# Performance work log

Measured on AMD Instinct MI355X. Metric: run time of the kernel, lower is better.

The kernel has to match this reference:

```python
import jax, jax.numpy as jnp
import numpy as np

EPS = 1e-5

def ln(x, g, b):
    m = x.mean(-1, keepdims=True)
    v = x.var(-1, keepdims=True)
    return (x - m) / jnp.sqrt(v + EPS) * g + b

def setup_inputs() -> dict:
    key = jax.random.key(0)
    ks = jax.random.split(key, 16)
    def p(k, shape, fan):
        return jax.random.normal(k, shape, jnp.float32) * (1.0 / np.sqrt(fan))
    B, N, M = 4, 256, 256
    C = 256
    inp = {}
    inp["tracks"] = jax.random.normal(ks[0], (B, 1028, N), jnp.float32)
    inp["detections"] = jax.random.normal(ks[1], (B, 1028, M), jnp.float32)
    # app encoder: Linear(1024,256) -> LN -> ReLU -> Linear(256,256)
    inp["wa1"] = p(ks[2], (1024, C), 1024); inp["ba1"] = jnp.zeros((C,), jnp.float32)
    inp["gla"] = jnp.ones((C,), jnp.float32); inp["bla"] = jnp.zeros((C,), jnp.float32)
    inp["wa2"] = p(ks[3], (C, C), C); inp["ba2"] = jnp.zeros((C,), jnp.float32)
    # geo encoder: Linear(4,128) -> LN -> ReLU -> Linear(128,256)
    inp["wg1"] = p(ks[4], (4, C // 2), 4); inp["bg1"] = jnp.zeros((C // 2,), jnp.float32)
    inp["glg"] = jnp.ones((C // 2,), jnp.float32); inp["blg"] = jnp.zeros((C // 2,), jnp.float32)
    inp["wg2"] = p(ks[5], (C // 2, C), C // 2); inp["bg2"] = jnp.zeros((C,), jnp.float32)
    # fusion LayerNorm
    inp["gf"] = jnp.ones((C,), jnp.float32); inp["bf"] = jnp.zeros((C,), jnp.float32)
    # cross-attention (4 heads, head_dim 64)
    inp["wq"] = p(ks[6], (C, C), C); inp["bq"] = jnp.zeros((C,), jnp.float32)
    inp["wk"] = p(ks[7], (C, C), C); inp["bk"] = jnp.zeros((C,), jnp.float32)
    inp["wv"] = p(ks[8], (C, C), C); inp["bv"] = jnp.zeros((C,), jnp.float32)
    inp["wo"] = p(ks[9], (C, C), C); inp["bo"] = jnp.zeros((C,), jnp.float32)
    # classifier: Linear(512,128) -> ReLU -> Linear(128,1)
    inp["wc1"] = p(ks[10], (2 * C, 128), 2 * C); inp["bc1"] = jnp.zeros((128,), jnp.float32)
    inp["wc2"] = p(ks[11], (128, 1), 128); inp["bc2"] = jnp.zeros((1,), jnp.float32)
    return inp

def reference(tracks, detections, wa1, ba1, gla, bla, wa2, ba2,
              wg1, bg1, glg, blg, wg2, bg2, gf, bf,
              wq, bq, wk, bk, wv, bv, wo, bo,
              wc1, bc1, wc2, bc2):
    tr = tracks.transpose(0, 2, 1)       # (B, N, 1028)
    de = detections.transpose(0, 2, 1)   # (B, M, 1028)

    def encode(x):
        app, geo = x[..., :1024], x[..., 1024:]
        h = jax.nn.relu(ln(app @ wa1 + ba1, gla, bla)) @ wa2 + ba2
        g = jax.nn.relu(ln(geo @ wg1 + bg1, glg, blg)) @ wg2 + bg2
        return ln(h + g, gf, bf)

    t_emb = encode(tr)   # (B, N, C)
    d_emb = encode(de)   # (B, M, C)

    B, N, C = t_emb.shape
    M = d_emb.shape[1]
    H, dh = 4, C // 4

    # Cross-attention (computed in the original forward but its output is never used)
    q = (t_emb @ wq + bq).reshape(B, N, H, dh)
    k = (d_emb @ wk + bk).reshape(B, M, H, dh)
    v = (d_emb @ wv + bv).reshape(B, M, H, dh)
    att = jax.nn.softmax(jnp.einsum('bnhd,bmhd->bhnm', q, k) / jnp.sqrt(jnp.float32(dh)), axis=-1)
    attn_out = jnp.einsum('bhnm,bmhd->bnhd', att, v).reshape(B, N, C) @ wo + bo  # unused, as in original

    # Pairwise classifier. cat([t_rep, d_rep], -1) @ wc1 == t @ wc1[:C] + d @ wc1[C:]
    a = t_emb @ wc1[:C]   # (B, N, 128)
    c = d_emb @ wc1[C:]   # (B, M, 128)
    h = jax.nn.relu(a[:, :, None, :] + c[:, None, :, :] + bc1)  # (B, N, M, 128)
    logits = (h @ wc2 + bc2)[..., 0]  # (B, N, M)
    return logits
```

## Files before the change

### kernel.cpp

```cpp
#include <hip/hip_runtime.h>

#define EPS 1e-5f


__global__ __launch_bounds__(256) void k_gemm1(
    const float* __restrict__ tracks, const float* __restrict__ dets,
    const float* __restrict__ wa1, float* __restrict__ part)
{
    __shared__ float xs[128 * 16];
    const int blk = blockIdx.x;
    const int rt  = blk >> 3;
    const int ksi = blk & 7;
    const int g0  = rt * 16;
    const int side = g0 >> 10, b = (g0 >> 8) & 3, n0 = g0 & 255;
    const float* xb = (side ? dets : tracks) + (size_t)b * (1028 * 256);
    const int k0 = ksi * 128;
    const int tid = threadIdx.x;
    const int w   = tid >> 6;
    const int c0  = (tid & 63) * 4;

    for (int idx = tid; idx < 2048; idx += 256) {
        int f = idx >> 4, r = idx & 15;
        xs[f * 16 + r] = xb[(size_t)(k0 + f) * 256 + n0 + r];
    }
    __syncthreads();

    float acc[4][4];
#pragma unroll
    for (int i = 0; i < 4; ++i)
#pragma unroll
        for (int j = 0; j < 4; ++j) acc[i][j] = 0.f;

#pragma unroll 2
    for (int f = 0; f < 128; ++f) {
        float4 xv = *(const float4*)(xs + f * 16 + w * 4);
        float4 wv = *(const float4*)(wa1 + (size_t)(k0 + f) * 256 + c0);
        acc[0][0] = fmaf(xv.x, wv.x, acc[0][0]);
        acc[0][1] = fmaf(xv.x, wv.y, acc[0][1]);
        acc[0][2] = fmaf(xv.x, wv.z, acc[0][2]);
        acc[0][3] = fmaf(xv.x, wv.w, acc[0][3]);
        acc[1][0] = fmaf(xv.y, wv.x, acc[1][0]);
        acc[1][1] = fmaf(xv.y, wv.y, acc[1][1]);
        acc[1][2] = fmaf(xv.y, wv.z, acc[1][2]);
        acc[1][3] = fmaf(xv.y, wv.w, acc[1][3]);
        acc[2][0] = fmaf(xv.z, wv.x, acc[2][0]);
        acc[2][1] = fmaf(xv.z, wv.y, acc[2][1]);
        acc[2][2] = fmaf(xv.z, wv.z, acc[2][2]);
        acc[2][3] = fmaf(xv.z, wv.w, acc[2][3]);
        acc[3][0] = fmaf(xv.w, wv.x, acc[3][0]);
        acc[3][1] = fmaf(xv.w, wv.y, acc[3][1]);
        acc[3][2] = fmaf(xv.w, wv.z, acc[3][2]);
        acc[3][3] = fmaf(xv.w, wv.w, acc[3][3]);
    }
    float* pb = part + ((size_t)ksi * 2048 + g0 + w * 4) * 256 + c0;
#pragma unroll
    for (int i = 0; i < 4; ++i)
        *(float4*)(pb + (size_t)i * 256) =
            make_float4(acc[i][0], acc[i][1], acc[i][2], acc[i][3]);
}

__global__ __launch_bounds__(256) void k_reduce1(
    const float* __restrict__ tracks, const float* __restrict__ dets,
    const float* __restrict__ part,
    const float* __restrict__ ba1, const float* __restrict__ gla,
    const float* __restrict__ bla,
    const float* __restrict__ wg1, const float* __restrict__ bg1,
    const float* __restrict__ glg, const float* __restrict__ blg,
    float* __restrict__ h1ext)
{
    __shared__ float red[4][4][2];
    __shared__ float geo_s[4][4];
    const int blk = blockIdx.x;
    const int g0 = blk * 4;
    const int side = g0 >> 10, b = (g0 >> 8) & 3, n0 = g0 & 255;
    const float* xb = (side ? dets : tracks) + (size_t)b * (1028 * 256);
    const int tid = threadIdx.x, wave = tid >> 6, lane = tid & 63, c = tid;

    if (tid < 16)
        geo_s[tid >> 2][tid & 3] =
            xb[(size_t)(1024 + (tid & 3)) * 256 + n0 + (tid >> 2)];

    float h[4];
#pragma unroll
    for (int i = 0; i < 4; ++i) {
        float s = ba1[c];
#pragma unroll
        for (int s8 = 0; s8 < 8; ++s8)
            s += part[((size_t)s8 * 2048 + g0 + i) * 256 + c];
        h[i] = s;
    }
#pragma unroll
    for (int i = 0; i < 4; ++i) {
        float s = h[i], s2 = h[i] * h[i];
#pragma unroll
        for (int off = 32; off >= 1; off >>= 1) {
            s  += __shfl_xor(s,  off, 64);
            s2 += __shfl_xor(s2, off, 64);
        }
        if (lane == 0) { red[wave][i][0] = s; red[wave][i][1] = s2; }
    }
    __syncthreads();
    {
        float gv = gla[c], bv = bla[c];
#pragma unroll
        for (int i = 0; i < 4; ++i) {
            float s  = red[0][i][0] + red[1][i][0] + red[2][i][0] + red[3][i][0];
            float s2 = red[0][i][1] + red[1][i][1] + red[2][i][1] + red[3][i][1];
            float m   = s * (1.f / 256.f);
            float var = s2 * (1.f / 256.f) - m * m;
            h1ext[(size_t)(g0 + i) * 384 + c] =
                fmaxf((h[i] - m) * rsqrtf(var + EPS) * gv + bv, 0.f);
        }
    }
    __syncthreads();

    float gh[4];
    if (tid < 128) {
        const int j = tid;
#pragma unroll
        for (int i = 0; i < 4; ++i) {
            float s = bg1[j];
#pragma unroll
            for (int f = 0; f < 4; ++f)
                s = fmaf(geo_s[i][f], wg1[f * 128 + j], s);
            gh[i] = s;
        }
#pragma unroll
        for (int i = 0; i < 4; ++i) {
            float s = gh[i], s2 = gh[i] * gh[i];
#pragma unroll
            for (int off = 32; off >= 1; off >>= 1) {
                s  += __shfl_xor(s,  off, 64);
                s2 += __shfl_xor(s2, off, 64);
            }
            if (lane == 0) { red[wave][i][0] = s; red[wave][i][1] = s2; }
        }
    }
    __syncthreads();
    if (tid < 128) {
        const int j = tid;
        float gv = glg[j], bv = blg[j];
#pragma unroll
        for (int i = 0; i < 4; ++i) {
            float s  = red[0][i][0] + red[1][i][0];
            float s2 = red[0][i][1] + red[1][i][1];
            float m   = s * (1.f / 128.f);
            float var = s2 * (1.f / 128.f) - m * m;
            h1ext[(size_t)(g0 + i) * 384 + 256 + j] =
                fmaxf((gh[i] - m) * rsqrtf(var + EPS) * gv + bv, 0.f);
        }
    }
}

__global__ __launch_bounds__(256) void k_gemm2(
    const float* __restrict__ h1ext,
    const float* __restrict__ wa2, const float* __restrict__ wg2,
    float* __restrict__ part)
{
    __shared__ float xs[64 * 16];
    const int blk = blockIdx.x;
    const int rt = blk / 6, sl = blk - rt * 6;
    const int g0 = rt * 16;
    const int k0 = sl * 64;
    const int tid = threadIdx.x;
    const int w   = tid >> 6;
    const int c0  = (tid & 63) * 4;
    const float* Wb = (k0 < 256) ? (wa2 + (size_t)k0 * 256)
                                 : (wg2 + (size_t)(k0 - 256) * 256);

    for (int idx = tid; idx < 1024; idx += 256) {
        int f = idx >> 4, r = idx & 15;
        xs[f * 16 + r] = h1ext[(size_t)(g0 + r) * 384 + k0 + f];
    }
    __syncthreads();

    float acc[4][4];
#pragma unroll
    for (int i = 0; i < 4; ++i)
#pragma unroll
        for (int j = 0; j < 4; ++j) acc[i][j] = 0.f;

#pragma unroll 2
    for (int f = 0; f < 64; ++f) {
        float4 xv = *(const float4*)(xs + f * 16 + w * 4);
        float4 wv = *(const float4*)(Wb + (size_t)f * 256 + c0);
        acc[0][0] = fmaf(xv.x, wv.x, acc[0][0]);
        acc[0][1] = fmaf(xv.x, wv.y, acc[0][1]);
        acc[0][2] = fmaf(xv.x, wv.z, acc[0][2]);
        acc[0][3] = fmaf(xv.x, wv.w, acc[0][3]);
        acc[1][0] = fmaf(xv.y, wv.x, acc[1][0]);
        acc[1][1] = fmaf(xv.y, wv.y, acc[1][1]);
        acc[1][2] = fmaf(xv.y, wv.z, acc[1][2]);
        acc[1][3] = fmaf(xv.y, wv.w, acc[1][3]);
        acc[2][0] = fmaf(xv.z, wv.x, acc[2][0]);
        acc[2][1] = fmaf(xv.z, wv.y, acc[2][1]);
        acc[2][2] = fmaf(xv.z, wv.z, acc[2][2]);
        acc[2][3] = fmaf(xv.z, wv.w, acc[2][3]);
        acc[3][0] = fmaf(xv.w, wv.x, acc[3][0]);
        acc[3][1] = fmaf(xv.w, wv.y, acc[3][1]);
        acc[3][2] = fmaf(xv.w, wv.z, acc[3][2]);
        acc[3][3] = fmaf(xv.w, wv.w, acc[3][3]);
    }
    float* pb = part + ((size_t)sl * 2048 + g0 + w * 4) * 256 + c0;
#pragma unroll
    for (int i = 0; i < 4; ++i)
        *(float4*)(pb + (size_t)i * 256) =
            make_float4(acc[i][0], acc[i][1], acc[i][2], acc[i][3]);
}

__global__ __launch_bounds__(256) void k_reduce2(
    const float* __restrict__ part,
    const float* __restrict__ ba2, const float* __restrict__ bg2,
    const float* __restrict__ gf,  const float* __restrict__ bf,
    const float* __restrict__ wc1,
    float* __restrict__ aout, float* __restrict__ cout)
{
    __shared__ float red[4][4][2];
    __shared__ float emb[256 * 4];
    __shared__ float psum[2][4][128];
    const int blk = blockIdx.x;
    const int g0 = blk * 4;
    const int side = g0 >> 10, b = (g0 >> 8) & 3, nin = g0 & 255;
    const int tid = threadIdx.x, wave = tid >> 6, lane = tid & 63, c = tid;

    float h2[4];
#pragma unroll
    for (int i = 0; i < 4; ++i) {
        float s = ba2[c] + bg2[c];
#pragma unroll
        for (int sl = 0; sl < 6; ++sl)
            s += part[((size_t)sl * 2048 + g0 + i) * 256 + c];
        h2[i] = s;
    }
#pragma unroll
    for (int i = 0; i < 4; ++i) {
        float s = h2[i], s2 = h2[i] * h2[i];
#pragma unroll
        for (int off = 32; off >= 1; off >>= 1) {
            s  += __shfl_xor(s,  off, 64);
            s2 += __shfl_xor(s2, off, 64);
        }
        if (lane == 0) { red[wave][i][0] = s; red[wave][i][1] = s2; }
    }
    __syncthreads();
    {
        float gv = gf[c], bv = bf[c];
        float e[4];
#pragma unroll
        for (int i = 0; i < 4; ++i) {
            float s  = red[0][i][0] + red[1][i][0] + red[2][i][0] + red[3][i][0];
            float s2 = red[0][i][1] + red[1][i][1] + red[2][i][1] + red[3][i][1];
            float m   = s * (1.f / 256.f);
            float var = s2 * (1.f / 256.f) - m * m;
            e[i] = (h2[i] - m) * rsqrtf(var + EPS) * gv + bv;
        }
        *(float4*)(emb + (size_t)c * 4) = make_float4(e[0], e[1], e[2], e[3]);
    }
    __syncthreads();

    const int half = tid >> 7, j = tid & 127;
    const float* wch = wc1 + (size_t)side * (256 * 128);
    float a4[4] = {0.f, 0.f, 0.f, 0.f};
#pragma unroll 4
    for (int k = 0; k < 128; ++k) {
        int kk = half * 128 + k;
        float w = wch[(size_t)kk * 128 + j];
        float4 ev = *(const float4*)(emb + kk * 4);
        a4[0] = fmaf(ev.x, w, a4[0]); a4[1] = fmaf(ev.y, w, a4[1]);
        a4[2] = fmaf(ev.z, w, a4[2]); a4[3] = fmaf(ev.w, w, a4[3]);
    }
#pragma unroll
    for (int i = 0; i < 4; ++i) psum[half][i][j] = a4[i];
    __syncthreads();

    float* outp = (side ? cout : aout) + ((size_t)b * 256 + nin) * 128;
    for (int idx = tid; idx < 512; idx += 256) {
        int i = idx >> 7, jo = idx & 127;
        outp[(size_t)i * 128 + jo] = psum[0][i][jo] + psum[1][i][jo];
    }
}

__global__ __launch_bounds__(256) void k_pairwise(
    const float* __restrict__ a, const float* __restrict__ cmat,
    const float* __restrict__ bc1, const float* __restrict__ wc2,
    const float* __restrict__ bc2, float* __restrict__ out)
{
    __shared__ float4 a_s[32 * 33];
    __shared__ float4 c_s[32 * 33];
    const int blk = blockIdx.x;
    const int b  = blk >> 6;
    const int n0 = ((blk >> 3) & 7) << 5;
    const int m0 = (blk & 7) << 5;
    const int tid = threadIdx.x;

    const float4* a4  = (const float4*)(a    + ((size_t)b * 256 + n0) * 128);
    const float4* c4  = (const float4*)(cmat + ((size_t)b * 256 + m0) * 128);
    const float4* b14 = (const float4*)bc1;
    for (int idx = tid; idx < 1024; idx += 256) {
        int r = idx >> 5, q = idx & 31;
        float4 av = a4[r * 32 + q], bv = b14[q];
        a_s[r * 33 + q] = make_float4(av.x + bv.x, av.y + bv.y,
                                      av.z + bv.z, av.w + bv.w);
        c_s[r * 33 + q] = c4[r * 32 + q];
    }
    __syncthreads();

    const int ni = tid >> 4, mi = tid & 15;
    const float4* wp = (const float4*)wc2;
    float s00 = 0.f, s01 = 0.f, s10 = 0.f, s11 = 0.f;
#pragma unroll 4
    for (int q = 0; q < 32; ++q) {
        float4 av0 = a_s[ni * 33 + q];
        float4 av1 = a_s[(ni + 16) * 33 + q];
        float4 cv0 = c_s[mi * 33 + q];
        float4 cv1 = c_s[(mi + 16) * 33 + q];
        float4 wv  = wp[q];
        s00 = fmaf(fmaxf(av0.x + cv0.x, 0.f), wv.x, s00);
        s00 = fmaf(fmaxf(av0.y + cv0.y, 0.f), wv.y, s00);
        s00 = fmaf(fmaxf(av0.z + cv0.z, 0.f), wv.z, s00);
        s00 = fmaf(fmaxf(av0.w + cv0.w, 0.f), wv.w, s00);
        s01 = fmaf(fmaxf(av0.x + cv1.x, 0.f), wv.x, s01);
        s01 = fmaf(fmaxf(av0.y + cv1.y, 0.f), wv.y, s01);
        s01 = fmaf(fmaxf(av0.z + cv1.z, 0.f), wv.z, s01);
        s01 = fmaf(fmaxf(av0.w + cv1.w, 0.f), wv.w, s01);
        s10 = fmaf(fmaxf(av1.x + cv0.x, 0.f), wv.x, s10);
        s10 = fmaf(fmaxf(av1.y + cv0.y, 0.f), wv.y, s10);
        s10 = fmaf(fmaxf(av1.z + cv0.z, 0.f), wv.z, s10);
        s10 = fmaf(fmaxf(av1.w + cv0.w, 0.f), wv.w, s10);
        s11 = fmaf(fmaxf(av1.x + cv1.x, 0.f), wv.x, s11);
        s11 = fmaf(fmaxf(av1.y + cv1.y, 0.f), wv.y, s11);
        s11 = fmaf(fmaxf(av1.z + cv1.z, 0.f), wv.z, s11);
        s11 = fmaf(fmaxf(av1.w + cv1.w, 0.f), wv.w, s11);
    }
    const float b2 = bc2[0];
    float* ob = out + ((size_t)b * 256 + n0) * 256 + m0;
    ob[(size_t)ni * 256 + mi]               = s00 + b2;
    ob[(size_t)ni * 256 + mi + 16]          = s01 + b2;
    ob[(size_t)(ni + 16) * 256 + mi]        = s10 + b2;
    ob[(size_t)(ni + 16) * 256 + mi + 16]   = s11 + b2;
}

extern "C" void kernel_launch(void* const* d_in, const int* in_sizes, int n_in,
                              void* d_out, int out_size, void* d_ws, size_t ws_size,
                              hipStream_t stream)
{
    const float* tracks = (const float*)d_in[0];
    const float* dets   = (const float*)d_in[1];
    const float* wa1 = (const float*)d_in[2];
    const float* ba1 = (const float*)d_in[3];
    const float* gla = (const float*)d_in[4];
    const float* bla = (const float*)d_in[5];
    const float* wa2 = (const float*)d_in[6];
    const float* ba2 = (const float*)d_in[7];
    const float* wg1 = (const float*)d_in[8];
    const float* bg1 = (const float*)d_in[9];
    const float* glg = (const float*)d_in[10];
    const float* blg = (const float*)d_in[11];
    const float* wg2 = (const float*)d_in[12];
    const float* bg2 = (const float*)d_in[13];
    const float* gf  = (const float*)d_in[14];
    const float* bf  = (const float*)d_in[15];
    const float* wc1 = (const float*)d_in[24];
    const float* bc1 = (const float*)d_in[25];
    const float* wc2 = (const float*)d_in[26];
    const float* bc2 = (const float*)d_in[27];
    float* out = (float*)d_out;
    float* ws  = (float*)d_ws;

    float* part  = ws;
    float* h1ext = ws + 4194304;
    float* aa    = ws + 4980736;
    float* cc    = ws + 5111808;

    hipLaunchKernelGGL(k_gemm1, dim3(1024), dim3(256), 0, stream,
                       tracks, dets, wa1, part);
    hipLaunchKernelGGL(k_reduce1, dim3(512), dim3(256), 0, stream,
                       tracks, dets, part, ba1, gla, bla,
                       wg1, bg1, glg, blg, h1ext);
    hipLaunchKernelGGL(k_gemm2, dim3(768), dim3(256), 0, stream,
                       h1ext, wa2, wg2, part);
    hipLaunchKernelGGL(k_reduce2, dim3(512), dim3(256), 0, stream,
                       part, ba2, bg2, gf, bf, wc1, aa, cc);
    hipLaunchKernelGGL(k_pairwise, dim3(256), dim3(256), 0, stream,
                       aa, cc, bc1, wc2, bc2, out);
}
```

Before: 177.7 us.

## Prefetch weight tiles in registers for encoder GEMMs and shrink pairwise tiles

In both encoder GEMM kernels, weight rows are now loaded into a two-stage register buffer eight rows ahead, so global load latency overlaps with the FMAs. The launch bound also asks for four blocks per CU. The gemm1 input staging now uses float4 loads. The pairwise kernel moves from 32x32 tiles with a 2x2 output per thread to 16x16 tiles with one output per thread, quadrupling the grid to 1024 blocks for more parallelism, at the cost of less reuse of the a/c rows loaded into shared memory.

```diff
diff --git a/kernel.cpp b/kernel.cpp
--- a/kernel.cpp
+++ b/kernel.cpp
@@ -3,7 +3,7 @@
 #define EPS 1e-5f
 
 
-__global__ __launch_bounds__(256) void k_gemm1(
+__global__ __launch_bounds__(256, 4) void k_gemm1(
     const float* __restrict__ tracks, const float* __restrict__ dets,
     const float* __restrict__ wa1, float* __restrict__ part)
 {
@@ -19,9 +19,10 @@
     const int w   = tid >> 6;
     const int c0  = (tid & 63) * 4;
 
-    for (int idx = tid; idx < 2048; idx += 256) {
-        int f = idx >> 4, r = idx & 15;
-        xs[f * 16 + r] = xb[(size_t)(k0 + f) * 256 + n0 + r];
+    for (int t = tid; t < 512; t += 256) {
+        int f = t >> 2, r4 = (t & 3) << 2;
+        *(float4*)(xs + f * 16 + r4) =
+            *(const float4*)(xb + (size_t)(k0 + f) * 256 + n0 + r4);
     }
     __syncthreads();
 
@@ -31,26 +32,43 @@
 #pragma unroll
         for (int j = 0; j < 4; ++j) acc[i][j] = 0.f;
 
-#pragma unroll 2
-    for (int f = 0; f < 128; ++f) {
-        float4 xv = *(const float4*)(xs + f * 16 + w * 4);
-        float4 wv = *(const float4*)(wa1 + (size_t)(k0 + f) * 256 + c0);
-        acc[0][0] = fmaf(xv.x, wv.x, acc[0][0]);
-        acc[0][1] = fmaf(xv.x, wv.y, acc[0][1]);
-        acc[0][2] = fmaf(xv.x, wv.z, acc[0][2]);
-        acc[0][3] = fmaf(xv.x, wv.w, acc[0][3]);
-        acc[1][0] = fmaf(xv.y, wv.x, acc[1][0]);
-        acc[1][1] = fmaf(xv.y, wv.y, acc[1][1]);
-        acc[1][2] = fmaf(xv.y, wv.z, acc[1][2]);
-        acc[1][3] = fmaf(xv.y, wv.w, acc[1][3]);
-        acc[2][0] = fmaf(xv.z, wv.x, acc[2][0]);
-        acc[2][1] = fmaf(xv.z, wv.y, acc[2][1]);
-        acc[2][2] = fmaf(xv.z, wv.z, acc[2][2]);
-        acc[2][3] = fmaf(xv.z, wv.w, acc[2][3]);
-        acc[3][0] = fmaf(xv.w, wv.x, acc[3][0]);
-        acc[3][1] = fmaf(xv.w, wv.y, acc[3][1]);
-        acc[3][2] = fmaf(xv.w, wv.z, acc[3][2]);
-        acc[3][3] = fmaf(xv.w, wv.w, acc[3][3]);
+    const float* wptr = wa1 + (size_t)k0 * 256 + c0;
+    float4 wb[2][8];
+#pragma unroll
+    for (int j = 0; j < 8; ++j)
+        wb[0][j] = *(const float4*)(wptr + (size_t)j * 256);
+
+#pragma unroll
+    for (int bb = 0; bb < 16; ++bb) {
+        const int cur = bb & 1, nxt = cur ^ 1;
+        if (bb < 15) {
+#pragma unroll
+            for (int j = 0; j < 8; ++j)
+                wb[nxt][j] =
+                    *(const float4*)(wptr + (size_t)((bb + 1) * 8 + j) * 256);
+        }
+#pragma unroll
+        for (int j = 0; j < 8; ++j) {
+            const int f = bb * 8 + j;
+            float4 xv = *(const float4*)(xs + f * 16 + w * 4);
+            float4 wv = wb[cur][j];
+            acc[0][0] = fmaf(xv.x, wv.x, acc[0][0]);
+            acc[0][1] = fmaf(xv.x, wv.y, acc[0][1]);
+            acc[0][2] = fmaf(xv.x, wv.z, acc[0][2]);
+            acc[0][3] = fmaf(xv.x, wv.w, acc[0][3]);
+            acc[1][0] = fmaf(xv.y, wv.x, acc[1][0]);
+            acc[1][1] = fmaf(xv.y, wv.y, acc[1][1]);
+            acc[1][2] = fmaf(xv.y, wv.z, acc[1][2]);
+            acc[1][3] = fmaf(xv.y, wv.w, acc[1][3]);
+            acc[2][0] = fmaf(xv.z, wv.x, acc[2][0]);
+            acc[2][1] = fmaf(xv.z, wv.y, acc[2][1]);
+            acc[2][2] = fmaf(xv.z, wv.z, acc[2][2]);
+            acc[2][3] = fmaf(xv.z, wv.w, acc[2][3]);
+            acc[3][0] = fmaf(xv.w, wv.x, acc[3][0]);
+            acc[3][1] = fmaf(xv.w, wv.y, acc[3][1]);
+            acc[3][2] = fmaf(xv.w, wv.z, acc[3][2]);
+            acc[3][3] = fmaf(xv.w, wv.w, acc[3][3]);
+        }
     }
     float* pb = part + ((size_t)ksi * 2048 + g0 + w * 4) * 256 + c0;
 #pragma unroll
@@ -152,7 +170,7 @@
     }
 }
 
-__global__ __launch_bounds__(256) void k_gemm2(
+__global__ __launch_bounds__(256, 4) void k_gemm2(
     const float* __restrict__ h1ext,
     const float* __restrict__ wa2, const float* __restrict__ wg2,
     float* __restrict__ part)
@@ -180,26 +198,43 @@
 #pragma unroll
         for (int j = 0; j < 4; ++j) acc[i][j] = 0.f;
 
-#pragma unroll 2
-    for (int f = 0; f < 64; ++f) {
-        float4 xv = *(const float4*)(xs + f * 16 + w * 4);
-        float4 wv = *(const float4*)(Wb + (size_t)f * 256 + c0);
-        acc[0][0] = fmaf(xv.x, wv.x, acc[0][0]);
-        acc[0][1] = fmaf(xv.x, wv.y, acc[0][1]);
-        acc[0][2] = fmaf(xv.x, wv.z, acc[0][2]);
-        acc[0][3] = fmaf(xv.x, wv.w, acc[0][3]);
-        acc[1][0] = fmaf(xv.y, wv.x, acc[1][0]);
-        acc[1][1] = fmaf(xv.y, wv.y, acc[1][1]);
-        acc[1][2] = fmaf(xv.y, wv.z, acc[1][2]);
-        acc[1][3] = fmaf(xv.y, wv.w, acc[1][3]);
-        acc[2][0] = fmaf(xv.z, wv.x, acc[2][0]);
-        acc[2][1] = fmaf(xv.z, wv.y, acc[2][1]);
-        acc[2][2] = fmaf(xv.z, wv.z, acc[2][2]);
-        acc[2][3] = fmaf(xv.z, wv.w, acc[2][3]);
-        acc[3][0] = fmaf(xv.w, wv.x, acc[3][0]);
-        acc[3][1] = fmaf(xv.w, wv.y, acc[3][1]);
-        acc[3][2] = fmaf(xv.w, wv.z, acc[3][2]);
-        acc[3][3] = fmaf(xv.w, wv.w, acc[3][3]);
+    const float* wptr = Wb + c0;
+    float4 wb[2][8];
+#pragma unroll
+    for (int j = 0; j < 8; ++j)
+        wb[0][j] = *(const float4*)(wptr + (size_t)j * 256);
+
+#pragma unroll
+    for (int bb = 0; bb < 8; ++bb) {
+        const int cur = bb & 1, nxt = cur ^ 1;
+        if (bb < 7) {
+#pragma unroll
+            for (int j = 0; j < 8; ++j)
+                wb[nxt][j] =
+                    *(const float4*)(wptr + (size_t)((bb + 1) * 8 + j) * 256);
+        }
+#pragma unroll
+        for (int j = 0; j < 8; ++j) {
+            const int f = bb * 8 + j;
+            float4 xv = *(const float4*)(xs + f * 16 + w * 4);
+            float4 wv = wb[cur][j];
+            acc[0][0] = fmaf(xv.x, wv.x, acc[0][0]);
+            acc[0][1] = fmaf(xv.x, wv.y, acc[0][1]);
+            acc[0][2] = fmaf(xv.x, wv.z, acc[0][2]);
+            acc[0][3] = fmaf(xv.x, wv.w, acc[0][3]);
+            acc[1][0] = fmaf(xv.y, wv.x, acc[1][0]);
+            acc[1][1] = fmaf(xv.y, wv.y, acc[1][1]);
+            acc[1][2] = fmaf(xv.y, wv.z, acc[1][2]);
+            acc[1][3] = fmaf(xv.y, wv.w, acc[1][3]);
+            acc[2][0] = fmaf(xv.z, wv.x, acc[2][0]);
+            acc[2][1] = fmaf(xv.z, wv.y, acc[2][1]);
+            acc[2][2] = fmaf(xv.z, wv.z, acc[2][2]);
+            acc[2][3] = fmaf(xv.z, wv.w, acc[2][3]);
+            acc[3][0] = fmaf(xv.w, wv.x, acc[3][0]);
+            acc[3][1] = fmaf(xv.w, wv.y, acc[3][1]);
+            acc[3][2] = fmaf(xv.w, wv.z, acc[3][2]);
+            acc[3][3] = fmaf(xv.w, wv.w, acc[3][3]);
+        }
     }
     float* pb = part + ((size_t)sl * 2048 + g0 + w * 4) * 256 + c0;
 #pragma unroll
@@ -285,18 +320,18 @@
     const float* __restrict__ bc1, const float* __restrict__ wc2,
     const float* __restrict__ bc2, float* __restrict__ out)
 {
-    __shared__ float4 a_s[32 * 33];
-    __shared__ float4 c_s[32 * 33];
+    __shared__ float4 a_s[16 * 33];
+    __shared__ float4 c_s[16 * 33];
     const int blk = blockIdx.x;
-    const int b  = blk >> 6;
-    const int n0 = ((blk >> 3) & 7) << 5;
-    const int m0 = (blk & 7) << 5;
+    const int b  = blk >> 8;
+    const int n0 = ((blk >> 4) & 15) << 4;
+    const int m0 = (blk & 15) << 4;
     const int tid = threadIdx.x;
 
     const float4* a4  = (const float4*)(a    + ((size_t)b * 256 + n0) * 128);
     const float4* c4  = (const float4*)(cmat + ((size_t)b * 256 + m0) * 128);
     const float4* b14 = (const float4*)bc1;
-    for (int idx = tid; idx < 1024; idx += 256) {
+    for (int idx = tid; idx < 512; idx += 256) {
         int r = idx >> 5, q = idx & 31;
         float4 av = a4[r * 32 + q], bv = b14[q];
         a_s[r * 33 + q] = make_float4(av.x + bv.x, av.y + bv.y,
@@ -307,37 +342,18 @@
 
     const int ni = tid >> 4, mi = tid & 15;
     const float4* wp = (const float4*)wc2;
-    float s00 = 0.f, s01 = 0.f, s10 = 0.f, s11 = 0.f;
-#pragma unroll 4
+    float acc = bc2[0];
+#pragma unroll 8
     for (int q = 0; q < 32; ++q) {
-        float4 av0 = a_s[ni * 33 + q];
-        float4 av1 = a_s[(ni + 16) * 33 + q];
-        float4 cv0 = c_s[mi * 33 + q];
-        float4 cv1 = c_s[(mi + 16) * 33 + q];
-        float4 wv  = wp[q];
-        s00 = fmaf(fmaxf(av0.x + cv0.x, 0.f), wv.x, s00);
-        s00 = fmaf(fmaxf(av0.y + cv0.y, 0.f), wv.y, s00);
-        s00 = fmaf(fmaxf(av0.z + cv0.z, 0.f), wv.z, s00);
-        s00 = fmaf(fmaxf(av0.w + cv0.w, 0.f), wv.w, s00);
-        s01 = fmaf(fmaxf(av0.x + cv1.x, 0.f), wv.x, s01);
-        s01 = fmaf(fmaxf(av0.y + cv1.y, 0.f), wv.y, s01);
-        s01 = fmaf(fmaxf(av0.z + cv1.z, 0.f), wv.z, s01);
-        s01 = fmaf(fmaxf(av0.w + cv1.w, 0.f), wv.w, s01);
-        s10 = fmaf(fmaxf(av1.x + cv0.x, 0.f), wv.x, s10);
-        s10 = fmaf(fmaxf(av1.y + cv0.y, 0.f), wv.y, s10);
-        s10 = fmaf(fmaxf(av1.z + cv0.z, 0.f), wv.z, s10);
-        s10 = fmaf(fmaxf(av1.w + cv0.w, 0.f), wv.w, s10);
-        s11 = fmaf(fmaxf(av1.x + cv1.x, 0.f), wv.x, s11);
-        s11 = fmaf(fmaxf(av1.y + cv1.y, 0.f), wv.y, s11);
-        s11 = fmaf(fmaxf(av1.z + cv1.z, 0.f), wv.z, s11);
-        s11 = fmaf(fmaxf(av1.w + cv1.w, 0.f), wv.w, s11);
-    }
-    const float b2 = bc2[0];
-    float* ob = out + ((size_t)b * 256 + n0) * 256 + m0;
-    ob[(size_t)ni * 256 + mi]               = s00 + b2;
-    ob[(size_t)ni * 256 + mi + 16]          = s01 + b2;
-    ob[(size_t)(ni + 16) * 256 + mi]        = s10 + b2;
-    ob[(size_t)(ni + 16) * 256 + mi + 16]   = s11 + b2;
+        float4 av = a_s[ni * 33 + q];
+        float4 cv = c_s[mi * 33 + q];
+        float4 wv = wp[q];
+        acc = fmaf(fmaxf(av.x + cv.x, 0.f), wv.x, acc);
+        acc = fmaf(fmaxf(av.y + cv.y, 0.f), wv.y, acc);
+        acc = fmaf(fmaxf(av.z + cv.z, 0.f), wv.z, acc);
+        acc = fmaf(fmaxf(av.w + cv.w, 0.f), wv.w, acc);
+    }
+    out[((size_t)b * 256 + n0 + ni) * 256 + m0 + mi] = acc;
 }
 
 extern "C" void kernel_launch(void* const* d_in, const int* in_sizes, int n_in,
@@ -381,6 +397,6 @@
                        h1ext, wa2, wg2, part);
     hipLaunchKernelGGL(k_reduce2, dim3(512), dim3(256), 0, stream,
                        part, ba2, bg2, gf, bf, wc1, aa, cc);
-    hipLaunchKernelGGL(k_pairwise, dim3(256), dim3(256), 0, stream,
+    hipLaunchKernelGGL(k_pairwise, dim3(1024), dim3(256), 0, stream,
                        aa, cc, bc1, wc2, bc2, out);
 }
```

Result: faster. 169.0 us (-4.9%).
